# Kernel tuning notes

Measured on AMD Instinct MI355X. Metric: run time of the kernel, lower is better.

The kernel has to match this reference:

```python
import jax, jax.numpy as jnp
import numpy as np
import math

B, N0, DEG = 32, 1584, 4
E = B * N0 * DEG
FIN, HID, EDIM, ROUTE, HEADS = 32, 64, 8, 16, 4
NEG = 0.2  # leaky_relu negative slope (alpha)
K1 = math.ceil(0.8 * N0)   # 1268 nodes/graph after pool1
K2 = math.ceil(0.8 * K1)   # 1015 after pool2
K3 = math.ceil(0.8 * K2)   # 812 after pool3


def _gatv2(x, src, dst, emask, edge_attr, Wl, bl, Wr, br, We, att, bo, num_nodes):
    # PyG GATv2Conv, concat=False (mean over heads), edge_dim, eval mode (no dropout)
    xl = (x @ Wl + bl).reshape(-1, HEADS, HID)            # source transform  [N,H,C]
    xr = (x @ Wr + br).reshape(-1, HEADS, HID)            # target transform  [N,H,C]
    ee = (edge_attr @ We).reshape(-1, HEADS, HID)         # edge transform    [E,H,C]
    m = jax.nn.leaky_relu(xl[src] + xr[dst] + ee, NEG)    # [E,H,C]
    logits = jnp.einsum('ehc,hc->eh', m, att)             # [E,H]
    logits = jnp.where(emask[:, None], logits, -jnp.inf)
    mx = jax.ops.segment_max(logits, dst, num_segments=num_nodes)
    mx = jnp.where(jnp.isfinite(mx), mx, 0.0)             # nodes w/o in-edges
    ex = jnp.where(emask[:, None], jnp.exp(logits - mx[dst]), 0.0)
    den = jax.ops.segment_sum(ex, dst, num_segments=num_nodes)
    alpha = ex / jnp.maximum(den[dst], 1e-16)             # segment softmax over dst
    out = jax.ops.segment_sum(alpha[:, :, None] * xl[src], dst, num_segments=num_nodes)
    return out.mean(axis=1) + bo                          # concat=False -> head mean


def _topk(x, src, dst, emask, w, n_per, k):
    # PyG TopKPooling(ratio=0.8): score = tanh(x.w/||w||); keep top-k per graph,
    # scale kept features by score; keep edges whose endpoints both survive.
    s = jnp.tanh((x @ w) / jnp.linalg.norm(w))            # [B*n_per]
    _, idx = jax.lax.top_k(s.reshape(B, n_per), k)        # [B,k]
    perm = (idx + jnp.arange(B)[:, None] * n_per).reshape(-1)
    x_new = x[perm] * s[perm][:, None]
    new_id = jnp.full((B * n_per,), -1, jnp.int32).at[perm].set(
        jnp.arange(B * k, dtype=jnp.int32))
    nsrc, ndst = new_id[src], new_id[dst]
    m = emask & (nsrc >= 0) & (ndst >= 0)
    return x_new, jnp.where(m, nsrc, 0), jnp.where(m, ndst, 0), m


def _readout(x, k):
    # global mean pool || global max pool (nodes are grouped per graph, k each)
    xb = x.reshape(B, k, HID)
    return jnp.concatenate([xb.mean(1), xb.max(1)], axis=1)


def _forward(x, edge_attr, edge_index,
             g1_Wl, g1_bl, g1_Wr, g1_br, g1_We, g1_att, g1_b,
             g2_Wl, g2_bl, g2_Wr, g2_br, g2_We, g2_att, g2_b,
             g3_Wl, g3_bl, g3_Wr, g3_br, g3_We, g3_att, g3_b,
             p1_w, p2_w, p3_w,
             fc1_W, fc1_b, fc2_W, fc2_b, fc3_W, fc3_b):
    src, dst = edge_index[0], edge_index[1]
    emask = jnp.ones((E,), bool)
    h = jax.nn.relu(_gatv2(x, src, dst, emask, edge_attr,
                           g1_Wl, g1_bl, g1_Wr, g1_br, g1_We, g1_att, g1_b, B * N0))
    h, src, dst, emask = _topk(h, src, dst, emask, p1_w, N0, K1)
    x1 = _readout(h, K1)
    h = jax.nn.relu(_gatv2(h, src, dst, emask, edge_attr,
                           g2_Wl, g2_bl, g2_Wr, g2_br, g2_We, g2_att, g2_b, B * K1))
    h, src, dst, emask = _topk(h, src, dst, emask, p2_w, K1, K2)
    x2 = _readout(h, K2)
    h = jax.nn.relu(_gatv2(h, src, dst, emask, edge_attr,
                           g3_Wl, g3_bl, g3_Wr, g3_br, g3_We, g3_att, g3_b, B * K2))
    h, src, dst, emask = _topk(h, src, dst, emask, p3_w, K2, K3)
    x3 = _readout(h, K3)
    r = x1 + x2 + x3                                      # [B, 2*HID]
    h = jax.nn.relu(r @ fc1_W + fc1_b)
    h = jax.nn.relu(h @ fc2_W + fc2_b)                    # dropout results unused in source
    return jax.nn.softmax(h @ fc3_W + fc3_b, axis=1)      # [B, ROUTE]


def setup_inputs() -> dict:
    key = jax.random.key(0)
    ks = iter(jax.random.split(key, 64))
    def nrm(shape, scale):
        return jax.random.normal(next(ks), shape, jnp.float32) * scale
    x = nrm((B * N0, FIN), 1.0)
    srcl = jax.random.randint(next(ks), (B, N0 * DEG), 0, N0)
    dstl = jax.random.randint(next(ks), (B, N0 * DEG), 0, N0)
    off = (jnp.arange(B) * N0)[:, None]
    edge_index = jnp.stack([(srcl + off).reshape(-1),
                            (dstl + off).reshape(-1)]).astype(jnp.int32)
    edge_attr = nrm((E, EDIM), 1.0)
    batch = jnp.repeat(jnp.arange(B, dtype=jnp.int32), N0)
    inp = {"x": x, "edge_attr": edge_attr, "edge_index": edge_index, "batch": batch}
    for li, fin in ((1, FIN), (2, HID), (3, HID)):
        g = 1.0 / np.sqrt(fin)
        inp[f"g{li}_Wl"] = nrm((fin, HEADS * HID), g)
        inp[f"g{li}_bl"] = nrm((HEADS * HID,), 0.02)
        inp[f"g{li}_Wr"] = nrm((fin, HEADS * HID), g)
        inp[f"g{li}_br"] = nrm((HEADS * HID,), 0.02)
        inp[f"g{li}_We"] = nrm((EDIM, HEADS * HID), 1.0 / np.sqrt(EDIM))
        inp[f"g{li}_att"] = nrm((HEADS, HID), 1.0 / np.sqrt(HID))
        inp[f"g{li}_b"] = nrm((HID,), 0.02)
    for li in (1, 2, 3):
        inp[f"p{li}_w"] = nrm((HID,), 1.0 / np.sqrt(HID))
    for fin, fout, nm in ((2 * HID, HID, "fc1"), (HID, HID, "fc2"), (HID, ROUTE, "fc3")):
        inp[f"{nm}_W"] = nrm((fin, fout), 1.0 / np.sqrt(fin))
        inp[f"{nm}_b"] = nrm((fout,), 0.02)
    return inp


def reference(x, edge_attr, edge_index, batch,
              g1_Wl, g1_bl, g1_Wr, g1_br, g1_We, g1_att, g1_b,
              g2_Wl, g2_bl, g2_Wr, g2_br, g2_We, g2_att, g2_b,
              g3_Wl, g3_bl, g3_Wr, g3_br, g3_We, g3_att, g3_b,
              p1_w, p2_w, p3_w,
              fc1_W, fc1_b, fc2_W, fc2_b, fc3_W, fc3_b):
    # batch is implicit: nodes are laid out grouped per graph with static sizes
    del batch
    return _forward(x, edge_attr, edge_index,
                    g1_Wl, g1_bl, g1_Wr, g1_br, g1_We, g1_att, g1_b,
                    g2_Wl, g2_bl, g2_Wr, g2_br, g2_We, g2_att, g2_b,
                    g3_Wl, g3_bl, g3_Wr, g3_br, g3_We, g3_att, g3_b,
                    p1_w, p2_w, p3_w,
                    fc1_W, fc1_b, fc2_W, fc2_b, fc3_W, fc3_b)
```

## Files before the change

### kernel.cpp

```cpp
#include <hip/hip_runtime.h>

typedef unsigned short u16;
typedef unsigned int u32;
typedef unsigned long long u64;

#define E_TOT 202752
#define NMAX  50688
#define HEADS 4
#define B_    32
#define MAXDEG 32
#define REMAP_Y 25

#define CDIV(a,b) (((a)+(b)-1)/(b))

__device__ __forceinline__ u32 ford(float f) {
  u32 u = __float_as_uint(f);
  return (u & 0x80000000u) ? ~u : (u | 0x80000000u);
}
__device__ __forceinline__ float ford_inv(u32 u) {
  u32 b = (u & 0x80000000u) ? (u ^ 0x80000000u) : ~u;
  return __uint_as_float(b);
}

template <int CTRL>
__device__ __forceinline__ float dpp_mov(float x) {
  return __int_as_float(__builtin_amdgcn_mov_dpp(__float_as_int(x), CTRL, 0xF, 0xF, false));
}
__device__ __forceinline__ float row16_sum(float v) {
  v += dpp_mov<0x121>(v);
  v += dpp_mov<0x122>(v);
  v += dpp_mov<0x124>(v);
  v += dpp_mov<0x128>(v);
  return v;
}

__device__ __forceinline__ u64 shfl_xor_u64(u64 v, int mask) {
  int lo = __shfl_xor((int)(u32)(v & 0xFFFFFFFFu), mask, 64);
  int hi = __shfl_xor((int)(u32)(v >> 32), mask, 64);
  return ((u64)(u32)hi << 32) | (u32)lo;
}

__global__ void k_edge_init_csr(const int* __restrict__ ei, int* __restrict__ src,
                                int* __restrict__ dst, int* __restrict__ em,
                                int* __restrict__ cnt, int* __restrict__ csr) {
  int e = blockIdx.x * blockDim.x + threadIdx.x;
  if (e >= E_TOT) return;
  int s = ei[e], d = ei[E_TOT + e];
  src[e] = s;
  dst[e] = d;
  em[e] = 1;
  int pos = atomicAdd(&cnt[d], 1);
  if (pos < MAXDEG) csr[d * MAXDEG + pos] = e;
}

template <int FIN>
__global__ void k_transform_t(const float* __restrict__ hin,
                              const float* __restrict__ Wl, const float* __restrict__ bl,
                              const float* __restrict__ Wr, const float* __restrict__ br,
                              float* __restrict__ xl, float* __restrict__ xr) {
  __shared__ float xs[FIN][20];
  int n0 = blockIdx.x * 16, j = threadIdx.x;
  for (int t = j; t < 16 * FIN; t += 256) {
    int nd = t >> (FIN == 32 ? 5 : 6), f = t & (FIN - 1);
    xs[f][nd] = hin[(size_t)(n0 + nd) * FIN + f];
  }
  __syncthreads();
  float al[16], ar[16];
  float blv = bl[j], brv = br[j];
#pragma unroll
  for (int t = 0; t < 16; ++t) { al[t] = blv; ar[t] = brv; }
  for (int i = 0; i < FIN; ++i) {
    float wl = Wl[i * 256 + j], wr = Wr[i * 256 + j];
    float4 x0 = *(const float4*)&xs[i][0];
    float4 x1 = *(const float4*)&xs[i][4];
    float4 x2 = *(const float4*)&xs[i][8];
    float4 x3 = *(const float4*)&xs[i][12];
    al[0]  += x0.x * wl; ar[0]  += x0.x * wr;
    al[1]  += x0.y * wl; ar[1]  += x0.y * wr;
    al[2]  += x0.z * wl; ar[2]  += x0.z * wr;
    al[3]  += x0.w * wl; ar[3]  += x0.w * wr;
    al[4]  += x1.x * wl; ar[4]  += x1.x * wr;
    al[5]  += x1.y * wl; ar[5]  += x1.y * wr;
    al[6]  += x1.z * wl; ar[6]  += x1.z * wr;
    al[7]  += x1.w * wl; ar[7]  += x1.w * wr;
    al[8]  += x2.x * wl; ar[8]  += x2.x * wr;
    al[9]  += x2.y * wl; ar[9]  += x2.y * wr;
    al[10] += x2.z * wl; ar[10] += x2.z * wr;
    al[11] += x2.w * wl; ar[11] += x2.w * wr;
    al[12] += x3.x * wl; ar[12] += x3.x * wr;
    al[13] += x3.y * wl; ar[13] += x3.y * wr;
    al[14] += x3.z * wl; ar[14] += x3.z * wr;
    al[15] += x3.w * wl; ar[15] += x3.w * wr;
  }
#pragma unroll
  for (int t = 0; t < 16; ++t) {
    xl[(size_t)(n0 + t) * 256 + j] = al[t];
    xr[(size_t)(n0 + t) * 256 + j] = ar[t];
  }
}

__global__ void k_gat_fused(const int* __restrict__ srcv, const int* __restrict__ cnt,
                            const int* __restrict__ csr, const float* __restrict__ ea,
                            const float* __restrict__ We, const float* __restrict__ att,
                            const float* __restrict__ xl, const float* __restrict__ xr,
                            const float* __restrict__ bias, const float* __restrict__ pwv,
                            float* __restrict__ out, float* __restrict__ sc,
                            int n_per) {
  int b = blockIdx.x;
  int xcd = b & 7;
  int jj = b >> 3;
  int g = xcd + 8 * (jj >> 6);
  int wv = ((jj & 63) << 2) + (threadIdx.x >> 6);
  int lane = threadIdx.x & 63;
  int cg = lane & 15;
  int cb = (lane >> 4) * 64 + cg * 4;
  int npw = CDIV(n_per, 256);
  int l0 = wv * npw, l1 = min(n_per, l0 + npw);
  if (l0 >= n_per) return;
  int n0 = g * n_per + l0, n1 = g * n_per + l1;
  float4 at4 = *(const float4*)(att + cb);
  float4 w0 = *(const float4*)(We + 0 * 256 + cb);
  float4 w1 = *(const float4*)(We + 1 * 256 + cb);
  float4 w2 = *(const float4*)(We + 2 * 256 + cb);
  float4 w3 = *(const float4*)(We + 3 * 256 + cb);
  float4 w4_ = *(const float4*)(We + 4 * 256 + cb);
  float4 w5 = *(const float4*)(We + 5 * 256 + cb);
  float4 w6 = *(const float4*)(We + 6 * 256 + cb);
  float4 w7 = *(const float4*)(We + 7 * 256 + cb);
  float4 bi4 = *(const float4*)(bias + cg * 4);
  float4 pw4 = *(const float4*)(pwv + cg * 4);
  float wn = pw4.x * pw4.x + pw4.y * pw4.y + pw4.z * pw4.z + pw4.w * pw4.w;
  wn += __shfl_xor(wn, 1, 64); wn += __shfl_xor(wn, 2, 64);
  wn += __shfl_xor(wn, 4, 64); wn += __shfl_xor(wn, 8, 64);
  float isq = 1.f / sqrtf(wn);

  int degc = cnt[n0];
  int e_c = (lane < MAXDEG) ? csr[n0 * MAXDEG + lane] : 0;
  int s_c = srcv[e_c];
  float4 xdc = *(const float4*)(xr + (size_t)n0 * 256 + cb);

  for (int n = n0; n < n1; ++n) {
    int degn = 0, e_n = 0, s_n = 0;
    float4 xdn = xdc;
    if (n + 1 < n1) {
      degn = cnt[n + 1];
      e_n = (lane < MAXDEG) ? csr[(n + 1) * MAXDEG + lane] : 0;
      s_n = srcv[e_n];
      xdn = *(const float4*)(xr + (size_t)(n + 1) * 256 + cb);
    }
    int deg = min(degc, MAXDEG);
    int e_l = e_c, s_l = s_c;
    float4 xd4 = xdc;
    float m = -INFINITY, l = 0.f;
    float ox = 0.f, oy = 0.f, oz = 0.f, ow = 0.f;
    for (int i0 = 0; i0 < deg; i0 += 4) {
      int c0 = deg - i0; if (c0 > 4) c0 = 4;
      float4 xs[4], a0[4], a1[4];
#pragma unroll
      for (int j = 0; j < 4; ++j) {
        int idx = (j < c0) ? (i0 + j) : i0;
        int e = __builtin_amdgcn_readlane(e_l, idx);
        int s = __builtin_amdgcn_readlane(s_l, idx);
        xs[j] = *(const float4*)(xl + (size_t)s * 256 + cb);
        a0[j] = *(const float4*)(ea + (size_t)e * 8);
        a1[j] = *(const float4*)(ea + (size_t)e * 8 + 4);
      }
      float v[4];
#pragma unroll
      for (int j = 0; j < 4; ++j) {
        if (j < c0) {
          float e0 = a0[j].x * w0.x + a0[j].y * w1.x + a0[j].z * w2.x + a0[j].w * w3.x
                   + a1[j].x * w4_.x + a1[j].y * w5.x + a1[j].z * w6.x + a1[j].w * w7.x;
          float e1 = a0[j].x * w0.y + a0[j].y * w1.y + a0[j].z * w2.y + a0[j].w * w3.y
                   + a1[j].x * w4_.y + a1[j].y * w5.y + a1[j].z * w6.y + a1[j].w * w7.y;
          float e2 = a0[j].x * w0.z + a0[j].y * w1.z + a0[j].z * w2.z + a0[j].w * w3.z
                   + a1[j].x * w4_.z + a1[j].y * w5.z + a1[j].z * w6.z + a1[j].w * w7.z;
          float e3 = a0[j].x * w0.w + a0[j].y * w1.w + a0[j].z * w2.w + a0[j].w * w3.w
                   + a1[j].x * w4_.w + a1[j].y * w5.w + a1[j].z * w6.w + a1[j].w * w7.w;
          float m0 = xs[j].x + xd4.x + e0; m0 = (m0 >= 0.f) ? m0 : 0.2f * m0;
          float m1 = xs[j].y + xd4.y + e1; m1 = (m1 >= 0.f) ? m1 : 0.2f * m1;
          float m2 = xs[j].z + xd4.z + e2; m2 = (m2 >= 0.f) ? m2 : 0.2f * m2;
          float m3 = xs[j].w + xd4.w + e3; m3 = (m3 >= 0.f) ? m3 : 0.2f * m3;
          float d = at4.x * m0 + at4.y * m1 + at4.z * m2 + at4.w * m3;
          v[j] = row16_sum(d);
        } else {
          v[j] = -INFINITY;
        }
      }
      float vm = fmaxf(fmaxf(v[0], v[1]), fmaxf(v[2], v[3]));
      float nm = fmaxf(m, vm);
      float scale = __expf(m - nm);
      float p0 = __expf(v[0] - nm), p1 = __expf(v[1] - nm);
      float p2 = __expf(v[2] - nm), p3 = __expf(v[3] - nm);
      ox = ox * scale + ((p0 * xs[0].x + p1 * xs[1].x) + (p2 * xs[2].x + p3 * xs[3].x));
      oy = oy * scale + ((p0 * xs[0].y + p1 * xs[1].y) + (p2 * xs[2].y + p3 * xs[3].y));
      oz = oz * scale + ((p0 * xs[0].z + p1 * xs[1].z) + (p2 * xs[2].z + p3 * xs[3].z));
      ow = ow * scale + ((p0 * xs[0].w + p1 * xs[1].w) + (p2 * xs[2].w + p3 * xs[3].w));
      l = l * scale + ((p0 + p1) + (p2 + p3));
      m = nm;
    }
    float inv = 0.25f / fmaxf(l, 1e-16f);
    float r0 = ox * inv, r1 = oy * inv, r2 = oz * inv, r3 = ow * inv;
    r0 += __shfl_xor(r0, 16, 64); r0 += __shfl_xor(r0, 32, 64);
    r1 += __shfl_xor(r1, 16, 64); r1 += __shfl_xor(r1, 32, 64);
    r2 += __shfl_xor(r2, 16, 64); r2 += __shfl_xor(r2, 32, 64);
    r3 += __shfl_xor(r3, 16, 64); r3 += __shfl_xor(r3, 32, 64);
    float rr0 = fmaxf(r0 + bi4.x, 0.f), rr1 = fmaxf(r1 + bi4.y, 0.f);
    float rr2 = fmaxf(r2 + bi4.z, 0.f), rr3 = fmaxf(r3 + bi4.w, 0.f);
    if (lane < 16) *(float4*)(out + (size_t)n * 64 + cg * 4) = float4{rr0, rr1, rr2, rr3};
    float dot = rr0 * pw4.x + rr1 * pw4.y + rr2 * pw4.z + rr3 * pw4.w;
    dot += __shfl_xor(dot, 1, 64);
    dot += __shfl_xor(dot, 2, 64);
    dot += __shfl_xor(dot, 4, 64);
    dot += __shfl_xor(dot, 8, 64);
    if (lane == 0) sc[n] = tanhf(dot * isq);
    degc = degn; e_c = e_n; s_c = s_n; xdc = xdn;
  }
}

__global__ __launch_bounds__(1024) void k_topk(const float* __restrict__ s, int n_per,
                                               int k,
                                               int* __restrict__ perm, int* __restrict__ new_id,
                                               int* __restrict__ cnt) {
  __shared__ u64 kv[2048];
  int b = blockIdx.x, t = threadIdx.x;
  int base = b * n_per;
  for (int i = t; i < n_per; i += 1024) new_id[base + i] = -1;
  for (int i = t; i < k; i += 1024) cnt[b * k + i] = 0;

  u64 e0, e1;
  {
    u32 sk0 = (t < n_per) ? ford(s[base + t]) : 0u;
    int i1 = t + 1024;
    u32 sk1 = (i1 < n_per) ? ford(s[base + i1]) : 0u;
    e0 = ((u64)sk0 << 32) | (u32)(0xFFFFFFFFu - (u32)t);
    e1 = ((u64)sk1 << 32) | (u32)(0xFFFFFFFFu - (u32)i1);
  }

  for (int kk = 2; kk <= 2048; kk <<= 1) {
    int j = kk >> 1;
    if (j == 1024) {
      u64 mx = e0 > e1 ? e0 : e1;
      u64 mn = e0 > e1 ? e1 : e0;
      e0 = mx; e1 = mn;
      j >>= 1;
    }
    for (; j >= 64; j >>= 1) {
      __syncthreads();
      kv[t] = e0; kv[t + 1024] = e1;
      __syncthreads();
      u64 p0 = kv[t ^ j], p1 = kv[(t + 1024) ^ j];
      int i1 = t + 1024;
      bool km0 = (((t  & kk) == 0) == ((t  & j) == 0));
      bool km1 = (((i1 & kk) == 0) == ((i1 & j) == 0));
      e0 = km0 ? (e0 > p0 ? e0 : p0) : (e0 < p0 ? e0 : p0);
      e1 = km1 ? (e1 > p1 ? e1 : p1) : (e1 < p1 ? e1 : p1);
    }
    for (; j >= 1; j >>= 1) {
      u64 p0 = shfl_xor_u64(e0, j);
      u64 p1 = shfl_xor_u64(e1, j);
      int i1 = t + 1024;
      bool km0 = (((t  & kk) == 0) == ((t  & j) == 0));
      bool km1 = (((i1 & kk) == 0) == ((i1 & j) == 0));
      e0 = km0 ? (e0 > p0 ? e0 : p0) : (e0 < p0 ? e0 : p0);
      e1 = km1 ? (e1 > p1 ? e1 : p1) : (e1 < p1 ? e1 : p1);
    }
  }

  if (t < k) {
    int old0 = (int)(0xFFFFFFFFu - (u32)(e0 & 0xFFFFFFFFu));
    perm[b * k + t] = base + old0;
    new_id[base + old0] = b * k + t;
  }
  int r1 = t + 1024;
  if (r1 < k) {
    int old1 = (int)(0xFFFFFFFFu - (u32)(e1 & 0xFFFFFFFFu));
    perm[b * k + r1] = base + old1;
    new_id[base + old1] = b * k + r1;
  }
}

__global__ void k_post(const float* __restrict__ hin, const float* __restrict__ s,
                       const int* __restrict__ perm, float* __restrict__ hout,
                       int k, int gather_rows,
                       float* __restrict__ rsum, u32* __restrict__ rmaxI,
                       int* __restrict__ src, int* __restrict__ dst, int* __restrict__ em,
                       const int* __restrict__ new_id, int* __restrict__ cnt,
                       int* __restrict__ csr, int do_remap) {
  __shared__ float ps[256], pm[256];
  int b = blockIdx.x, yy = blockIdx.y, t = threadIdx.x;
  if (yy < gather_rows) {
    int i = yy * 4 + (t >> 6);
    int c = t & 63;
    bool valid = i < k;
    float v = 0.f;
    if (valid) {
      int g = perm[b * k + i];
      v = hin[(size_t)g * 64 + c] * s[g];
      hout[((size_t)b * k + i) * 64 + c] = v;
    }
    ps[t] = valid ? v : 0.f;
    pm[t] = valid ? v : -INFINITY;
    __syncthreads();
    if (t < 64) {
      float s4 = ps[t] + ps[t + 64] + ps[t + 128] + ps[t + 192];
      float m4 = fmaxf(fmaxf(pm[t], pm[t + 64]), fmaxf(pm[t + 128], pm[t + 192]));
      atomicAdd(&rsum[b * 64 + t], s4);
      atomicMax(&rmaxI[b * 64 + t], ford(m4));
    }
  } else if (do_remap) {
    int e = ((yy - gather_rows) * 32 + b) * 256 + t;
    if (e < E_TOT) {
      int ns = new_id[src[e]], nd = new_id[dst[e]];
      int mm = em[e] && ns >= 0 && nd >= 0;
      src[e] = mm ? ns : 0;
      dst[e] = mm ? nd : 0;
      em[e] = mm;
      if (mm) {
        int pos = atomicAdd(&cnt[nd], 1);
        if (pos < MAXDEG) csr[nd * MAXDEG + pos] = e;
      }
    }
  }
}

__global__ void k_mlp(const char* __restrict__ rblk,
                      const float* __restrict__ W1, const float* __restrict__ b1,
                      const float* __restrict__ W2, const float* __restrict__ b2,
                      const float* __restrict__ W3, const float* __restrict__ b3,
                      float* __restrict__ out) {
  __shared__ float v0[128], v1[64], v2[64], lgts[16];
  int b = blockIdx.x, t = threadIdx.x;
  const float* rs0 = (const float*)rblk;
  const u32*   rm0 = (const u32*)(rblk + 32 * 64 * 4);
  const float* rs1 = (const float*)(rblk + 32 * 128 * 4);
  const u32*   rm1 = (const u32*)(rblk + 32 * 128 * 4 + 32 * 64 * 4);
  const float* rs2 = (const float*)(rblk + 2 * 32 * 128 * 4);
  const u32*   rm2 = (const u32*)(rblk + 2 * 32 * 128 * 4 + 32 * 64 * 4);
  v0[t] = rs0[b * 64 + t] / 1268.f + rs1[b * 64 + t] / 1015.f + rs2[b * 64 + t] / 812.f;
  v0[64 + t] = ford_inv(rm0[b * 64 + t]) + ford_inv(rm1[b * 64 + t]) + ford_inv(rm2[b * 64 + t]);
  __syncthreads();
  float a = b1[t];
  for (int i = 0; i < 128; ++i) a += v0[i] * W1[i * 64 + t];
  v1[t] = fmaxf(a, 0.f);
  __syncthreads();
  a = b2[t];
  for (int i = 0; i < 64; ++i) a += v1[i] * W2[i * 64 + t];
  v2[t] = fmaxf(a, 0.f);
  __syncthreads();
  if (t < 16) {
    a = b3[t];
    for (int i = 0; i < 64; ++i) a += v2[i] * W3[i * 16 + t];
    lgts[t] = a;
  }
  __syncthreads();
  if (t == 0) {
    float m = lgts[0];
    for (int j = 1; j < 16; ++j) m = fmaxf(m, lgts[j]);
    float ex[16], sum = 0.f;
    for (int j = 0; j < 16; ++j) { ex[j] = expf(lgts[j] - m); sum += ex[j]; }
    for (int j = 0; j < 16; ++j) out[b * 16 + j] = ex[j] / sum;
  }
}

extern "C" void kernel_launch(void* const* d_in, const int* in_sizes, int n_in,
                              void* d_out, int out_size, void* d_ws, size_t ws_size,
                              hipStream_t stream) {
  (void)in_sizes; (void)n_in; (void)out_size; (void)ws_size;
  const float* x  = (const float*)d_in[0];
  const float* ea = (const float*)d_in[1];
  const int*   ei = (const int*)d_in[2];

  const float *gWl[3], *gbl[3], *gWr[3], *gbr[3], *gWe[3], *gatt[3], *gb[3], *pw[3];
  for (int l = 0; l < 3; ++l) {
    int p0 = 4 + 7 * l;
    gWl[l]  = (const float*)d_in[p0 + 0];
    gbl[l]  = (const float*)d_in[p0 + 1];
    gWr[l]  = (const float*)d_in[p0 + 2];
    gbr[l]  = (const float*)d_in[p0 + 3];
    gWe[l]  = (const float*)d_in[p0 + 4];
    gatt[l] = (const float*)d_in[p0 + 5];
    gb[l]   = (const float*)d_in[p0 + 6];
    pw[l]   = (const float*)d_in[25 + l];
  }
  const float* fc1W = (const float*)d_in[28];
  const float* fc1b = (const float*)d_in[29];
  const float* fc2W = (const float*)d_in[30];
  const float* fc2b = (const float*)d_in[31];
  const float* fc3W = (const float*)d_in[32];
  const float* fc3b = (const float*)d_in[33];

  char* w = (char*)d_ws;
  size_t off = 0;
  auto alloc = [&](size_t bytes) -> void* {
    void* p = w + off;
    off += (bytes + 255) & ~(size_t)255;
    return p;
  };
  float* hbuf = (float*)alloc((size_t)B_ * 1268 * 64 * 4);
  float* xl   = (float*)alloc((size_t)NMAX * 256 * 4);
  float* xr   = (float*)alloc((size_t)NMAX * 256 * 4);
  float* nacc = (float*)alloc((size_t)NMAX * 64 * 4);
  int*   cnt  = (int*)alloc((size_t)NMAX * 4);
  char*  rblk = (char*)alloc(3 * 32 * 128 * 4);
  int*   csr  = (int*)alloc((size_t)NMAX * MAXDEG * 4);
  float* sbuf = (float*)alloc((size_t)NMAX * 4);
  int* src    = (int*)alloc((size_t)E_TOT * 4);
  int* dst    = (int*)alloc((size_t)E_TOT * 4);
  int* em     = (int*)alloc((size_t)E_TOT * 4);
  int* new_id = (int*)alloc((size_t)NMAX * 4);
  int* perm   = (int*)alloc((size_t)32 * 1268 * 4);

  hipMemsetAsync(cnt, 0, (size_t)NMAX * 4, stream);
  hipMemsetAsync(rblk, 0, 3 * 32 * 128 * 4, stream);
  hipMemsetAsync(csr, 0, (size_t)NMAX * MAXDEG * 4, stream);
  k_edge_init_csr<<<CDIV(E_TOT, 256), 256, 0, stream>>>(ei, src, dst, em, cnt, csr);

  const int Ns[3]    = {50688, 40576, 32480};
  const int npers[3] = {1584, 1268, 1015};
  const int ks[3]    = {1268, 1015, 812};
  const int GAT_BLOCKS = 2048;

  for (int l = 0; l < 3; ++l) {
    int N = Ns[l];
    const float* hin = (l == 0) ? x : hbuf;
    float* rsum = (float*)(rblk + l * 32 * 128 * 4);
    u32* rmaxI  = (u32*)(rblk + l * 32 * 128 * 4 + 32 * 64 * 4);
    if (l == 0)
      k_transform_t<32><<<N / 16, 256, 0, stream>>>(hin, gWl[l], gbl[l], gWr[l], gbr[l], xl, xr);
    else
      k_transform_t<64><<<N / 16, 256, 0, stream>>>(hin, gWl[l], gbl[l], gWr[l], gbr[l], xl, xr);
    k_gat_fused<<<GAT_BLOCKS, 256, 0, stream>>>(src, cnt, csr, ea, gWe[l], gatt[l],
                                                xl, xr, gb[l], pw[l], nacc, sbuf, npers[l]);
    k_topk<<<32, 1024, 0, stream>>>(sbuf, npers[l], ks[l], perm, new_id, cnt);
    int grows = CDIV(ks[l], 4);
    dim3 pgrid(32, grows + (l < 2 ? REMAP_Y : 0));
    k_post<<<pgrid, 256, 0, stream>>>(nacc, sbuf, perm, hbuf, ks[l], grows, rsum, rmaxI,
                                      src, dst, em, new_id, cnt, csr, (l < 2) ? 1 : 0);
  }
  k_mlp<<<32, 64, 0, stream>>>(rblk, fc1W, fc1b, fc2W, fc2b, fc3W, fc3b, (float*)d_out);
}
```

Measured before the change: 488.4 us.

## Fuse top-k selection, feature gather, readout and edge remap into one per-graph kernel

```diff
diff --git a/kernel.cpp b/kernel.cpp
--- a/kernel.cpp
+++ b/kernel.cpp
@@ -6,10 +6,10 @@
 
 #define E_TOT 202752
 #define NMAX  50688
+#define EPG   6336
 #define HEADS 4
 #define B_    32
 #define MAXDEG 32
-#define REMAP_Y 25
 
 #define CDIV(a,b) (((a)+(b)-1)/(b))
 
@@ -218,21 +218,24 @@
   }
 }
 
-__global__ __launch_bounds__(1024) void k_topk(const float* __restrict__ s, int n_per,
-                                               int k,
-                                               int* __restrict__ perm, int* __restrict__ new_id,
-                                               int* __restrict__ cnt) {
+__global__ __launch_bounds__(1024) void k_topk_fused(
+    const float* __restrict__ sc, const float* __restrict__ hin,
+    float* __restrict__ hout, float* __restrict__ rsum, u32* __restrict__ rmaxI,
+    int* __restrict__ src, int* __restrict__ dst, int* __restrict__ em,
+    int* __restrict__ cnt, int* __restrict__ csr,
+    int n_per, int k, int do_remap) {
   __shared__ u64 kv[2048];
+  __shared__ int nid[1600];
+  __shared__ float red[2048];
   int b = blockIdx.x, t = threadIdx.x;
   int base = b * n_per;
-  for (int i = t; i < n_per; i += 1024) new_id[base + i] = -1;
-  for (int i = t; i < k; i += 1024) cnt[b * k + i] = 0;
+  for (int i = t; i < n_per; i += 1024) nid[i] = -1;
 
   u64 e0, e1;
   {
-    u32 sk0 = (t < n_per) ? ford(s[base + t]) : 0u;
+    u32 sk0 = (t < n_per) ? ford(sc[base + t]) : 0u;
     int i1 = t + 1024;
-    u32 sk1 = (i1 < n_per) ? ford(s[base + i1]) : 0u;
+    u32 sk1 = (i1 < n_per) ? ford(sc[base + i1]) : 0u;
     e0 = ((u64)sk0 << 32) | (u32)(0xFFFFFFFFu - (u32)t);
     e1 = ((u64)sk1 << 32) | (u32)(0xFFFFFFFFu - (u32)i1);
   }
@@ -267,58 +270,62 @@
     }
   }
 
+  __syncthreads();
+  kv[t] = e0; kv[t + 1024] = e1;
   if (t < k) {
     int old0 = (int)(0xFFFFFFFFu - (u32)(e0 & 0xFFFFFFFFu));
-    perm[b * k + t] = base + old0;
-    new_id[base + old0] = b * k + t;
+    nid[old0] = t;
   }
   int r1 = t + 1024;
   if (r1 < k) {
     int old1 = (int)(0xFFFFFFFFu - (u32)(e1 & 0xFFFFFFFFu));
-    perm[b * k + r1] = base + old1;
-    new_id[base + old1] = b * k + r1;
-  }
-}
-
-__global__ void k_post(const float* __restrict__ hin, const float* __restrict__ s,
-                       const int* __restrict__ perm, float* __restrict__ hout,
-                       int k, int gather_rows,
-                       float* __restrict__ rsum, u32* __restrict__ rmaxI,
-                       int* __restrict__ src, int* __restrict__ dst, int* __restrict__ em,
-                       const int* __restrict__ new_id, int* __restrict__ cnt,
-                       int* __restrict__ csr, int do_remap) {
-  __shared__ float ps[256], pm[256];
-  int b = blockIdx.x, yy = blockIdx.y, t = threadIdx.x;
-  if (yy < gather_rows) {
-    int i = yy * 4 + (t >> 6);
+    nid[old1] = r1;
+  }
+  __syncthreads();
+
+  {
     int c = t & 63;
-    bool valid = i < k;
-    float v = 0.f;
-    if (valid) {
-      int g = perm[b * k + i];
-      v = hin[(size_t)g * 64 + c] * s[g];
+    float acc = 0.f, mx = -INFINITY;
+    for (int i = (t >> 6); i < k; i += 16) {
+      u64 kvi = kv[i];
+      int old = (int)(0xFFFFFFFFu - (u32)(kvi & 0xFFFFFFFFu));
+      float s = ford_inv((u32)(kvi >> 32));
+      float v = hin[(size_t)(base + old) * 64 + c] * s;
       hout[((size_t)b * k + i) * 64 + c] = v;
-    }
-    ps[t] = valid ? v : 0.f;
-    pm[t] = valid ? v : -INFINITY;
+      acc += v;
+      mx = fmaxf(mx, v);
+    }
+    red[t] = acc;
+    red[1024 + t] = mx;
+  }
+  __syncthreads();
+  if (t < 64) {
+    float s4 = 0.f, m4 = -INFINITY;
+#pragma unroll
+    for (int j = 0; j < 16; ++j) {
+      s4 += red[t + j * 64];
+      m4 = fmaxf(m4, red[1024 + t + j * 64]);
+    }
+    rsum[b * 64 + t] = s4;
+    rmaxI[b * 64 + t] = ford(m4);
+  }
+
+  if (do_remap) {
+    for (int i = t; i < k; i += 1024) cnt[b * k + i] = 0;
     __syncthreads();
-    if (t < 64) {
-      float s4 = ps[t] + ps[t + 64] + ps[t + 128] + ps[t + 192];
-      float m4 = fmaxf(fmaxf(pm[t], pm[t + 64]), fmaxf(pm[t + 128], pm[t + 192]));
-      atomicAdd(&rsum[b * 64 + t], s4);
-      atomicMax(&rmaxI[b * 64 + t], ford(m4));
-    }
-  } else if (do_remap) {
-    int e = ((yy - gather_rows) * 32 + b) * 256 + t;
-    if (e < E_TOT) {
-      int ns = new_id[src[e]], nd = new_id[dst[e]];
-      int mm = em[e] && ns >= 0 && nd >= 0;
-      src[e] = mm ? ns : 0;
-      dst[e] = mm ? nd : 0;
+    for (int e = b * EPG + t; e < (b + 1) * EPG; e += 1024) {
+      int mmE = em[e];
+      int osl = mmE ? (src[e] - base) : 0;
+      int odl = mmE ? (dst[e] - base) : 0;
+      int ns = nid[osl], nd2 = nid[odl];
+      int mm = mmE && ns >= 0 && nd2 >= 0;
+      src[e] = mm ? (b * k + ns) : 0;
+      dst[e] = mm ? (b * k + nd2) : 0;
       em[e] = mm;
       if (mm) {
-        int pos = atomicAdd(&cnt[nd], 1);
-        if (pos < MAXDEG) csr[nd * MAXDEG + pos] = e;
+        int gd = b * k + nd2;
+        int pos = atomicAdd(&cnt[gd], 1);
+        if (pos < MAXDEG) csr[gd * MAXDEG + pos] = e;
       }
     }
   }
@@ -408,12 +415,9 @@
   int* src    = (int*)alloc((size_t)E_TOT * 4);
   int* dst    = (int*)alloc((size_t)E_TOT * 4);
   int* em     = (int*)alloc((size_t)E_TOT * 4);
-  int* new_id = (int*)alloc((size_t)NMAX * 4);
-  int* perm   = (int*)alloc((size_t)32 * 1268 * 4);
-
-  hipMemsetAsync(cnt, 0, (size_t)NMAX * 4, stream);
-  hipMemsetAsync(rblk, 0, 3 * 32 * 128 * 4, stream);
-  hipMemsetAsync(csr, 0, (size_t)NMAX * MAXDEG * 4, stream);
+
+  size_t zbytes = (size_t)NMAX * 4 + 3 * 32 * 128 * 4 + (size_t)NMAX * MAXDEG * 4;
+  hipMemsetAsync(cnt, 0, zbytes, stream);
   k_edge_init_csr<<<CDIV(E_TOT, 256), 256, 0, stream>>>(ei, src, dst, em, cnt, csr);
 
   const int Ns[3]    = {50688, 40576, 32480};
@@ -432,11 +436,9 @@
       k_transform_t<64><<<N / 16, 256, 0, stream>>>(hin, gWl[l], gbl[l], gWr[l], gbr[l], xl, xr);
     k_gat_fused<<<GAT_BLOCKS, 256, 0, stream>>>(src, cnt, csr, ea, gWe[l], gatt[l],
                                                 xl, xr, gb[l], pw[l], nacc, sbuf, npers[l]);
-    k_topk<<<32, 1024, 0, stream>>>(sbuf, npers[l], ks[l], perm, new_id, cnt);
-    int grows = CDIV(ks[l], 4);
-    dim3 pgrid(32, grows + (l < 2 ? REMAP_Y : 0));
-    k_post<<<pgrid, 256, 0, stream>>>(nacc, sbuf, perm, hbuf, ks[l], grows, rsum, rmaxI,
-                                      src, dst, em, new_id, cnt, csr, (l < 2) ? 1 : 0);
+    k_topk_fused<<<32, 1024, 0, stream>>>(sbuf, nacc, hbuf, rsum, rmaxI,
+                                          src, dst, em, cnt, csr,
+                                          npers[l], ks[l], (l < 2) ? 1 : 0);
   }
   k_mlp<<<32, 64, 0, stream>>>(rblk, fc1W, fc1b, fc2W, fc2b, fc3W, fc3b, (float*)d_out);
 }
```

Measured after the change: 528.3 us. 1.08x slower.

## Prefetch first edge batch of next node and merge memsets into one

Applied to the files above, without the earlier changes.

```diff
diff --git a/kernel.cpp b/kernel.cpp
--- a/kernel.cpp
+++ b/kernel.cpp
@@ -134,53 +134,55 @@
   wn += __shfl_xor(wn, 4, 64); wn += __shfl_xor(wn, 8, 64);
   float isq = 1.f / sqrtf(wn);
 
-  int degc = cnt[n0];
-  int e_c = (lane < MAXDEG) ? csr[n0 * MAXDEG + lane] : 0;
-  int s_c = srcv[e_c];
-  float4 xdc = *(const float4*)(xr + (size_t)n0 * 256 + cb);
+  int np1 = min(n0 + 1, n1 - 1);
+  int deg_0 = cnt[n0];
+  int e0v = (lane < MAXDEG) ? csr[n0 * MAXDEG + lane] : 0;
+  int s0v = srcv[e0v];
+  float4 xd0 = *(const float4*)(xr + (size_t)n0 * 256 + cb);
+  int deg_1 = cnt[np1];
+  int e1v = (lane < MAXDEG) ? csr[np1 * MAXDEG + lane] : 0;
+  int s1v = srcv[e1v];
+  float4 xd1 = *(const float4*)(xr + (size_t)np1 * 256 + cb);
+  float4 pxs[4], pa0[4], pa1[4];
+#pragma unroll
+  for (int j = 0; j < 4; ++j) {
+    int ee = __builtin_amdgcn_readlane(e0v, j);
+    int ss = __builtin_amdgcn_readlane(s0v, j);
+    pxs[j] = *(const float4*)(xl + (size_t)ss * 256 + cb);
+    pa0[j] = *(const float4*)(ea + (size_t)ee * 8);
+    pa1[j] = *(const float4*)(ea + (size_t)ee * 8 + 4);
+  }
 
   for (int n = n0; n < n1; ++n) {
-    int degn = 0, e_n = 0, s_n = 0;
-    float4 xdn = xdc;
-    if (n + 1 < n1) {
-      degn = cnt[n + 1];
-      e_n = (lane < MAXDEG) ? csr[(n + 1) * MAXDEG + lane] : 0;
-      s_n = srcv[e_n];
-      xdn = *(const float4*)(xr + (size_t)(n + 1) * 256 + cb);
-    }
-    int deg = min(degc, MAXDEG);
-    int e_l = e_c, s_l = s_c;
-    float4 xd4 = xdc;
+    int np2 = min(n + 2, n1 - 1);
+    int deg_2 = cnt[np2];
+    int e2v = (lane < MAXDEG) ? csr[np2 * MAXDEG + lane] : 0;
+    int s2v = srcv[e2v];
+    float4 xd2 = *(const float4*)(xr + (size_t)np2 * 256 + cb);
+
+    int deg = min(deg_0, MAXDEG);
+    float4 xd4 = xd0;
     float m = -INFINITY, l = 0.f;
     float ox = 0.f, oy = 0.f, oz = 0.f, ow = 0.f;
-    for (int i0 = 0; i0 < deg; i0 += 4) {
-      int c0 = deg - i0; if (c0 > 4) c0 = 4;
-      float4 xs[4], a0[4], a1[4];
-#pragma unroll
-      for (int j = 0; j < 4; ++j) {
-        int idx = (j < c0) ? (i0 + j) : i0;
-        int e = __builtin_amdgcn_readlane(e_l, idx);
-        int s = __builtin_amdgcn_readlane(s_l, idx);
-        xs[j] = *(const float4*)(xl + (size_t)s * 256 + cb);
-        a0[j] = *(const float4*)(ea + (size_t)e * 8);
-        a1[j] = *(const float4*)(ea + (size_t)e * 8 + 4);
-      }
+
+    if (deg > 0) {
+      int c0 = deg < 4 ? deg : 4;
       float v[4];
 #pragma unroll
       for (int j = 0; j < 4; ++j) {
         if (j < c0) {
-          float e0 = a0[j].x * w0.x + a0[j].y * w1.x + a0[j].z * w2.x + a0[j].w * w3.x
-                   + a1[j].x * w4_.x + a1[j].y * w5.x + a1[j].z * w6.x + a1[j].w * w7.x;
-          float e1 = a0[j].x * w0.y + a0[j].y * w1.y + a0[j].z * w2.y + a0[j].w * w3.y
-                   + a1[j].x * w4_.y + a1[j].y * w5.y + a1[j].z * w6.y + a1[j].w * w7.y;
-          float e2 = a0[j].x * w0.z + a0[j].y * w1.z + a0[j].z * w2.z + a0[j].w * w3.z
-                   + a1[j].x * w4_.z + a1[j].y * w5.z + a1[j].z * w6.z + a1[j].w * w7.z;
-          float e3 = a0[j].x * w0.w + a0[j].y * w1.w + a0[j].z * w2.w + a0[j].w * w3.w
-                   + a1[j].x * w4_.w + a1[j].y * w5.w + a1[j].z * w6.w + a1[j].w * w7.w;
-          float m0 = xs[j].x + xd4.x + e0; m0 = (m0 >= 0.f) ? m0 : 0.2f * m0;
-          float m1 = xs[j].y + xd4.y + e1; m1 = (m1 >= 0.f) ? m1 : 0.2f * m1;
-          float m2 = xs[j].z + xd4.z + e2; m2 = (m2 >= 0.f) ? m2 : 0.2f * m2;
-          float m3 = xs[j].w + xd4.w + e3; m3 = (m3 >= 0.f) ? m3 : 0.2f * m3;
+          float e0 = pa0[j].x * w0.x + pa0[j].y * w1.x + pa0[j].z * w2.x + pa0[j].w * w3.x
+                   + pa1[j].x * w4_.x + pa1[j].y * w5.x + pa1[j].z * w6.x + pa1[j].w * w7.x;
+          float e1 = pa0[j].x * w0.y + pa0[j].y * w1.y + pa0[j].z * w2.y + pa0[j].w * w3.y
+                   + pa1[j].x * w4_.y + pa1[j].y * w5.y + pa1[j].z * w6.y + pa1[j].w * w7.y;
+          float e2 = pa0[j].x * w0.z + pa0[j].y * w1.z + pa0[j].z * w2.z + pa0[j].w * w3.z
+                   + pa1[j].x * w4_.z + pa1[j].y * w5.z + pa1[j].z * w6.z + pa1[j].w * w7.z;
+          float e3 = pa0[j].x * w0.w + pa0[j].y * w1.w + pa0[j].z * w2.w + pa0[j].w * w3.w
+                   + pa1[j].x * w4_.w + pa1[j].y * w5.w + pa1[j].z * w6.w + pa1[j].w * w7.w;
+          float m0 = pxs[j].x + xd4.x + e0; m0 = (m0 >= 0.f) ? m0 : 0.2f * m0;
+          float m1 = pxs[j].y + xd4.y + e1; m1 = (m1 >= 0.f) ? m1 : 0.2f * m1;
+          float m2 = pxs[j].z + xd4.z + e2; m2 = (m2 >= 0.f) ? m2 : 0.2f * m2;
+          float m3 = pxs[j].w + xd4.w + e3; m3 = (m3 >= 0.f) ? m3 : 0.2f * m3;
           float d = at4.x * m0 + at4.y * m1 + at4.z * m2 + at4.w * m3;
           v[j] = row16_sum(d);
         } else {
@@ -188,17 +190,72 @@
         }
       }
       float vm = fmaxf(fmaxf(v[0], v[1]), fmaxf(v[2], v[3]));
-      float nm = fmaxf(m, vm);
-      float scale = __expf(m - nm);
+      float nm = vm;
       float p0 = __expf(v[0] - nm), p1 = __expf(v[1] - nm);
       float p2 = __expf(v[2] - nm), p3 = __expf(v[3] - nm);
-      ox = ox * scale + ((p0 * xs[0].x + p1 * xs[1].x) + (p2 * xs[2].x + p3 * xs[3].x));
-      oy = oy * scale + ((p0 * xs[0].y + p1 * xs[1].y) + (p2 * xs[2].y + p3 * xs[3].y));
-      oz = oz * scale + ((p0 * xs[0].z + p1 * xs[1].z) + (p2 * xs[2].z + p3 * xs[3].z));
-      ow = ow * scale + ((p0 * xs[0].w + p1 * xs[1].w) + (p2 * xs[2].w + p3 * xs[3].w));
-      l = l * scale + ((p0 + p1) + (p2 + p3));
+      ox = (p0 * pxs[0].x + p1 * pxs[1].x) + (p2 * pxs[2].x + p3 * pxs[3].x);
+      oy = (p0 * pxs[0].y + p1 * pxs[1].y) + (p2 * pxs[2].y + p3 * pxs[3].y);
+      oz = (p0 * pxs[0].z + p1 * pxs[1].z) + (p2 * pxs[2].z + p3 * pxs[3].z);
+      ow = (p0 * pxs[0].w + p1 * pxs[1].w) + (p2 * pxs[2].w + p3 * pxs[3].w);
+      l = (p0 + p1) + (p2 + p3);
       m = nm;
-    }
+      for (int i0 = 4; i0 < deg; i0 += 4) {
+        int c0i = deg - i0; if (c0i > 4) c0i = 4;
+        float4 ixs[4], ia0[4], ia1[4];
+#pragma unroll
+        for (int j = 0; j < 4; ++j) {
+          int idx = (j < c0i) ? (i0 + j) : i0;
+          int e = __builtin_amdgcn_readlane(e0v, idx);
+          int s = __builtin_amdgcn_readlane(s0v, idx);
+          ixs[j] = *(const float4*)(xl + (size_t)s * 256 + cb);
+          ia0[j] = *(const float4*)(ea + (size_t)e * 8);
+          ia1[j] = *(const float4*)(ea + (size_t)e * 8 + 4);
+        }
+        float vv[4];
+#pragma unroll
+        for (int j = 0; j < 4; ++j) {
+          if (j < c0i) {
+            float e0 = ia0[j].x * w0.x + ia0[j].y * w1.x + ia0[j].z * w2.x + ia0[j].w * w3.x
+                     + ia1[j].x * w4_.x + ia1[j].y * w5.x + ia1[j].z * w6.x + ia1[j].w * w7.x;
+            float e1 = ia0[j].x * w0.y + ia0[j].y * w1.y + ia0[j].z * w2.y + ia0[j].w * w3.y
+                     + ia1[j].x * w4_.y + ia1[j].y * w5.y + ia1[j].z * w6.y + ia1[j].w * w7.y;
+            float e2 = ia0[j].x * w0.z + ia0[j].y * w1.z + ia0[j].z * w2.z + ia0[j].w * w3.z
+                     + ia1[j].x * w4_.z + ia1[j].y * w5.z + ia1[j].z * w6.z + ia1[j].w * w7.z;
+            float e3 = ia0[j].x * w0.w + ia0[j].y * w1.w + ia0[j].z * w2.w + ia0[j].w * w3.w
+                     + ia1[j].x * w4_.w + ia1[j].y * w5.w + ia1[j].z * w6.w + ia1[j].w * w7.w;
+            float m0 = ixs[j].x + xd4.x + e0; m0 = (m0 >= 0.f) ? m0 : 0.2f * m0;
+            float m1 = ixs[j].y + xd4.y + e1; m1 = (m1 >= 0.f) ? m1 : 0.2f * m1;
+            float m2 = ixs[j].z + xd4.z + e2; m2 = (m2 >= 0.f) ? m2 : 0.2f * m2;
+            float m3 = ixs[j].w + xd4.w + e3; m3 = (m3 >= 0.f) ? m3 : 0.2f * m3;
+            float d = at4.x * m0 + at4.y * m1 + at4.z * m2 + at4.w * m3;
+            vv[j] = row16_sum(d);
+          } else {
+            vv[j] = -INFINITY;
+          }
+        }
+        float vmi = fmaxf(fmaxf(vv[0], vv[1]), fmaxf(vv[2], vv[3]));
+        float nmi = fmaxf(m, vmi);
+        float scale = __expf(m - nmi);
+        float q0 = __expf(vv[0] - nmi), q1 = __expf(vv[1] - nmi);
+        float q2 = __expf(vv[2] - nmi), q3 = __expf(vv[3] - nmi);
+        ox = ox * scale + ((q0 * ixs[0].x + q1 * ixs[1].x) + (q2 * ixs[2].x + q3 * ixs[3].x));
+        oy = oy * scale + ((q0 * ixs[0].y + q1 * ixs[1].y) + (q2 * ixs[2].y + q3 * ixs[3].y));
+        oz = oz * scale + ((q0 * ixs[0].z + q1 * ixs[1].z) + (q2 * ixs[2].z + q3 * ixs[3].z));
+        ow = ow * scale + ((q0 * ixs[0].w + q1 * ixs[1].w) + (q2 * ixs[2].w + q3 * ixs[3].w));
+        l = l * scale + ((q0 + q1) + (q2 + q3));
+        m = nmi;
+      }
+    }
+
+#pragma unroll
+    for (int j = 0; j < 4; ++j) {
+      int ee = __builtin_amdgcn_readlane(e1v, j);
+      int ss = __builtin_amdgcn_readlane(s1v, j);
+      pxs[j] = *(const float4*)(xl + (size_t)ss * 256 + cb);
+      pa0[j] = *(const float4*)(ea + (size_t)ee * 8);
+      pa1[j] = *(const float4*)(ea + (size_t)ee * 8 + 4);
+    }
+
     float inv = 0.25f / fmaxf(l, 1e-16f);
     float r0 = ox * inv, r1 = oy * inv, r2 = oz * inv, r3 = ow * inv;
     r0 += __shfl_xor(r0, 16, 64); r0 += __shfl_xor(r0, 32, 64);
@@ -214,7 +271,9 @@
     dot += __shfl_xor(dot, 4, 64);
     dot += __shfl_xor(dot, 8, 64);
     if (lane == 0) sc[n] = tanhf(dot * isq);
-    degc = degn; e_c = e_n; s_c = s_n; xdc = xdn;
+
+    deg_0 = deg_1; e0v = e1v; s0v = s1v; xd0 = xd1;
+    deg_1 = deg_2; e1v = e2v; s1v = s2v; xd1 = xd2;
   }
 }
 
@@ -411,9 +470,8 @@
   int* new_id = (int*)alloc((size_t)NMAX * 4);
   int* perm   = (int*)alloc((size_t)32 * 1268 * 4);
 
-  hipMemsetAsync(cnt, 0, (size_t)NMAX * 4, stream);
-  hipMemsetAsync(rblk, 0, 3 * 32 * 128 * 4, stream);
-  hipMemsetAsync(csr, 0, (size_t)NMAX * MAXDEG * 4, stream);
+  size_t zbytes = (size_t)NMAX * 4 + 3 * 32 * 128 * 4 + (size_t)NMAX * MAXDEG * 4;
+  hipMemsetAsync(cnt, 0, zbytes, stream);
   k_edge_init_csr<<<CDIV(E_TOT, 256), 256, 0, stream>>>(ei, src, dst, em, cnt, csr);
 
   const int Ns[3]    = {50688, 40576, 32480};
```

Measured after the change: 521.9 us. 6.9% more time.

## Fuse top-k and pooling into one kernel with per-graph flag handoff

Applied to the files above, without the earlier changes.

```diff
diff --git a/kernel.cpp b/kernel.cpp
--- a/kernel.cpp
+++ b/kernel.cpp
@@ -6,10 +6,10 @@
 
 #define E_TOT 202752
 #define NMAX  50688
+#define EPG   6336
 #define HEADS 4
 #define B_    32
 #define MAXDEG 32
-#define REMAP_Y 25
 
 #define CDIV(a,b) (((a)+(b)-1)/(b))
 
@@ -218,99 +218,112 @@
   }
 }
 
-__global__ __launch_bounds__(1024) void k_topk(const float* __restrict__ s, int n_per,
-                                               int k,
-                                               int* __restrict__ perm, int* __restrict__ new_id,
-                                               int* __restrict__ cnt) {
+__global__ __launch_bounds__(1024) void k_pool(
+    const float* __restrict__ s, const float* __restrict__ hin, float* __restrict__ hout,
+    float* __restrict__ rsum, u32* __restrict__ rmaxI,
+    int* __restrict__ src, int* __restrict__ dst, int* __restrict__ em,
+    int* __restrict__ cnt, int* __restrict__ csr,
+    int* __restrict__ perm, int* __restrict__ new_id, int* __restrict__ flag,
+    int n_per, int k, int do_remap) {
   __shared__ u64 kv[2048];
-  int b = blockIdx.x, t = threadIdx.x;
+  int b = blockIdx.x, role = blockIdx.y, t = threadIdx.x;
   int base = b * n_per;
-  for (int i = t; i < n_per; i += 1024) new_id[base + i] = -1;
-  for (int i = t; i < k; i += 1024) cnt[b * k + i] = 0;
-
-  u64 e0, e1;
+
+  if (role == 0) {
+    for (int i = t; i < n_per; i += 1024) new_id[base + i] = -1;
+    for (int i = t; i < k; i += 1024) cnt[b * k + i] = 0;
+    u64 e0, e1;
+    {
+      u32 sk0 = (t < n_per) ? ford(s[base + t]) : 0u;
+      int i1 = t + 1024;
+      u32 sk1 = (i1 < n_per) ? ford(s[base + i1]) : 0u;
+      e0 = ((u64)sk0 << 32) | (u32)(0xFFFFFFFFu - (u32)t);
+      e1 = ((u64)sk1 << 32) | (u32)(0xFFFFFFFFu - (u32)i1);
+    }
+    for (int kk = 2; kk <= 2048; kk <<= 1) {
+      int j = kk >> 1;
+      if (j == 1024) {
+        u64 mx = e0 > e1 ? e0 : e1;
+        u64 mn = e0 > e1 ? e1 : e0;
+        e0 = mx; e1 = mn;
+        j >>= 1;
+      }
+      for (; j >= 64; j >>= 1) {
+        __syncthreads();
+        kv[t] = e0; kv[t + 1024] = e1;
+        __syncthreads();
+        u64 p0 = kv[t ^ j], p1 = kv[(t + 1024) ^ j];
+        int i1 = t + 1024;
+        bool km0 = (((t  & kk) == 0) == ((t  & j) == 0));
+        bool km1 = (((i1 & kk) == 0) == ((i1 & j) == 0));
+        e0 = km0 ? (e0 > p0 ? e0 : p0) : (e0 < p0 ? e0 : p0);
+        e1 = km1 ? (e1 > p1 ? e1 : p1) : (e1 < p1 ? e1 : p1);
+      }
+      for (; j >= 1; j >>= 1) {
+        u64 p0 = shfl_xor_u64(e0, j);
+        u64 p1 = shfl_xor_u64(e1, j);
+        int i1 = t + 1024;
+        bool km0 = (((t  & kk) == 0) == ((t  & j) == 0));
+        bool km1 = (((i1 & kk) == 0) == ((i1 & j) == 0));
+        e0 = km0 ? (e0 > p0 ? e0 : p0) : (e0 < p0 ? e0 : p0);
+        e1 = km1 ? (e1 > p1 ? e1 : p1) : (e1 < p1 ? e1 : p1);
+      }
+    }
+    if (t < k) {
+      int old0 = (int)(0xFFFFFFFFu - (u32)(e0 & 0xFFFFFFFFu));
+      perm[b * k + t] = base + old0;
+      new_id[base + old0] = b * k + t;
+    }
+    int r1 = t + 1024;
+    if (r1 < k) {
+      int old1 = (int)(0xFFFFFFFFu - (u32)(e1 & 0xFFFFFFFFu));
+      perm[b * k + r1] = base + old1;
+      new_id[base + old1] = b * k + r1;
+    }
+    __syncthreads();
+    __threadfence();
+    if (t == 0) atomicExch(&flag[b], 1);
+    return;
+  }
+
+  if (t == 0) {
+    while (atomicAdd(&flag[b], 0) == 0) { __builtin_amdgcn_s_sleep(8); }
+  }
+  __syncthreads();
+  __threadfence();
+
+  float* ps = (float*)kv;
+  float* pm = ps + 1024;
+  int slice = role - 1;
+  int per = CDIV(k, 15);
+  int i0 = slice * per, i1e = min(k, i0 + per);
   {
-    u32 sk0 = (t < n_per) ? ford(s[base + t]) : 0u;
-    int i1 = t + 1024;
-    u32 sk1 = (i1 < n_per) ? ford(s[base + i1]) : 0u;
-    e0 = ((u64)sk0 << 32) | (u32)(0xFFFFFFFFu - (u32)t);
-    e1 = ((u64)sk1 << 32) | (u32)(0xFFFFFFFFu - (u32)i1);
-  }
-
-  for (int kk = 2; kk <= 2048; kk <<= 1) {
-    int j = kk >> 1;
-    if (j == 1024) {
-      u64 mx = e0 > e1 ? e0 : e1;
-      u64 mn = e0 > e1 ? e1 : e0;
-      e0 = mx; e1 = mn;
-      j >>= 1;
-    }
-    for (; j >= 64; j >>= 1) {
-      __syncthreads();
-      kv[t] = e0; kv[t + 1024] = e1;
-      __syncthreads();
-      u64 p0 = kv[t ^ j], p1 = kv[(t + 1024) ^ j];
-      int i1 = t + 1024;
-      bool km0 = (((t  & kk) == 0) == ((t  & j) == 0));
-      bool km1 = (((i1 & kk) == 0) == ((i1 & j) == 0));
-      e0 = km0 ? (e0 > p0 ? e0 : p0) : (e0 < p0 ? e0 : p0);
-      e1 = km1 ? (e1 > p1 ? e1 : p1) : (e1 < p1 ? e1 : p1);
-    }
-    for (; j >= 1; j >>= 1) {
-      u64 p0 = shfl_xor_u64(e0, j);
-      u64 p1 = shfl_xor_u64(e1, j);
-      int i1 = t + 1024;
-      bool km0 = (((t  & kk) == 0) == ((t  & j) == 0));
-      bool km1 = (((i1 & kk) == 0) == ((i1 & j) == 0));
-      e0 = km0 ? (e0 > p0 ? e0 : p0) : (e0 < p0 ? e0 : p0);
-      e1 = km1 ? (e1 > p1 ? e1 : p1) : (e1 < p1 ? e1 : p1);
-    }
-  }
-
-  if (t < k) {
-    int old0 = (int)(0xFFFFFFFFu - (u32)(e0 & 0xFFFFFFFFu));
-    perm[b * k + t] = base + old0;
-    new_id[base + old0] = b * k + t;
-  }
-  int r1 = t + 1024;
-  if (r1 < k) {
-    int old1 = (int)(0xFFFFFFFFu - (u32)(e1 & 0xFFFFFFFFu));
-    perm[b * k + r1] = base + old1;
-    new_id[base + old1] = b * k + r1;
-  }
-}
-
-__global__ void k_post(const float* __restrict__ hin, const float* __restrict__ s,
-                       const int* __restrict__ perm, float* __restrict__ hout,
-                       int k, int gather_rows,
-                       float* __restrict__ rsum, u32* __restrict__ rmaxI,
-                       int* __restrict__ src, int* __restrict__ dst, int* __restrict__ em,
-                       const int* __restrict__ new_id, int* __restrict__ cnt,
-                       int* __restrict__ csr, int do_remap) {
-  __shared__ float ps[256], pm[256];
-  int b = blockIdx.x, yy = blockIdx.y, t = threadIdx.x;
-  if (yy < gather_rows) {
-    int i = yy * 4 + (t >> 6);
     int c = t & 63;
-    bool valid = i < k;
-    float v = 0.f;
-    if (valid) {
-      int g = perm[b * k + i];
-      v = hin[(size_t)g * 64 + c] * s[g];
+    float acc = 0.f, mx = -INFINITY;
+    for (int i = i0 + (t >> 6); i < i1e; i += 16) {
+      int gidx = perm[b * k + i];
+      float v = hin[(size_t)gidx * 64 + c] * s[gidx];
       hout[((size_t)b * k + i) * 64 + c] = v;
-    }
-    ps[t] = valid ? v : 0.f;
-    pm[t] = valid ? v : -INFINITY;
-    __syncthreads();
-    if (t < 64) {
-      float s4 = ps[t] + ps[t + 64] + ps[t + 128] + ps[t + 192];
-      float m4 = fmaxf(fmaxf(pm[t], pm[t + 64]), fmaxf(pm[t + 128], pm[t + 192]));
-      atomicAdd(&rsum[b * 64 + t], s4);
-      atomicMax(&rmaxI[b * 64 + t], ford(m4));
-    }
-  } else if (do_remap) {
-    int e = ((yy - gather_rows) * 32 + b) * 256 + t;
-    if (e < E_TOT) {
+      acc += v;
+      mx = fmaxf(mx, v);
+    }
+    ps[t] = acc;
+    pm[t] = mx;
+  }
+  __syncthreads();
+  if (t < 64) {
+    float s4 = 0.f, m4 = -INFINITY;
+#pragma unroll
+    for (int j = 0; j < 16; ++j) {
+      s4 += ps[t + j * 64];
+      m4 = fmaxf(m4, pm[t + j * 64]);
+    }
+    atomicAdd(&rsum[b * 64 + t], s4);
+    atomicMax(&rmaxI[b * 64 + t], ford(m4));
+  }
+
+  if (do_remap) {
+    for (int e = b * EPG + slice * 1024 + t; e < (b + 1) * EPG; e += 15 * 1024) {
       int ns = new_id[src[e]], nd = new_id[dst[e]];
       int mm = em[e] && ns >= 0 && nd >= 0;
       src[e] = mm ? ns : 0;
@@ -404,6 +417,7 @@
   int*   cnt  = (int*)alloc((size_t)NMAX * 4);
   char*  rblk = (char*)alloc(3 * 32 * 128 * 4);
   int*   csr  = (int*)alloc((size_t)NMAX * MAXDEG * 4);
+  int*   flags= (int*)alloc(3 * 32 * 4);
   float* sbuf = (float*)alloc((size_t)NMAX * 4);
   int* src    = (int*)alloc((size_t)E_TOT * 4);
   int* dst    = (int*)alloc((size_t)E_TOT * 4);
@@ -411,9 +425,9 @@
   int* new_id = (int*)alloc((size_t)NMAX * 4);
   int* perm   = (int*)alloc((size_t)32 * 1268 * 4);
 
-  hipMemsetAsync(cnt, 0, (size_t)NMAX * 4, stream);
-  hipMemsetAsync(rblk, 0, 3 * 32 * 128 * 4, stream);
-  hipMemsetAsync(csr, 0, (size_t)NMAX * MAXDEG * 4, stream);
+  size_t zbytes = (size_t)NMAX * 4 + 3 * 32 * 128 * 4 + (size_t)NMAX * MAXDEG * 4
+                + 256 ;
+  hipMemsetAsync(cnt, 0, zbytes, stream);
   k_edge_init_csr<<<CDIV(E_TOT, 256), 256, 0, stream>>>(ei, src, dst, em, cnt, csr);
 
   const int Ns[3]    = {50688, 40576, 32480};
@@ -432,11 +446,10 @@
       k_transform_t<64><<<N / 16, 256, 0, stream>>>(hin, gWl[l], gbl[l], gWr[l], gbr[l], xl, xr);
     k_gat_fused<<<GAT_BLOCKS, 256, 0, stream>>>(src, cnt, csr, ea, gWe[l], gatt[l],
                                                 xl, xr, gb[l], pw[l], nacc, sbuf, npers[l]);
-    k_topk<<<32, 1024, 0, stream>>>(sbuf, npers[l], ks[l], perm, new_id, cnt);
-    int grows = CDIV(ks[l], 4);
-    dim3 pgrid(32, grows + (l < 2 ? REMAP_Y : 0));
-    k_post<<<pgrid, 256, 0, stream>>>(nacc, sbuf, perm, hbuf, ks[l], grows, rsum, rmaxI,
-                                      src, dst, em, new_id, cnt, csr, (l < 2) ? 1 : 0);
+    k_pool<<<dim3(32, 16), 1024, 0, stream>>>(sbuf, nacc, hbuf, rsum, rmaxI,
+                                              src, dst, em, cnt, csr,
+                                              perm, new_id, flags + l * 32,
+                                              npers[l], ks[l], (l < 2) ? 1 : 0);
   }
   k_mlp<<<32, 64, 0, stream>>>(rblk, fc1W, fc1b, fc2W, fc2b, fc3W, fc3b, (float*)d_out);
 }
```

After: 804.4 us. +64.7%, slower.
